# Kernel tuning notes

Measured on AMD Instinct MI355X. Metric: run time of the kernel, lower is better.

## Reference

```python
import jax, jax.numpy as jnp
import numpy as np

D = 1024        # d_model
H = 16          # query heads
HKV = 4         # kv heads (GQA)
HD = D // H     # head dim = 64
MAX_T = 1024
EPS = 1e-6
CAP = 50.0      # logit softcap


def _rope_cache(max_t, hd):
    inv = 1.0 / (10000.0 ** (np.arange(0, hd, 2, dtype=np.float32) / hd))  # (hd/2,)
    t = np.arange(max_t, dtype=np.float32)
    f = np.outer(t, inv)                                                   # (max_t, hd/2)
    return jnp.asarray(np.cos(f)), jnp.asarray(np.sin(f))


def setup_inputs() -> dict:
    key = jax.random.key(0)
    ks = jax.random.split(key, 5)
    x = jax.random.normal(ks[0], (2, 64, 256, D), jnp.float32)  # (B,T,S,D)
    wq = jax.random.normal(ks[1], (D, H * HD), jnp.float32) * 0.02
    wk = jax.random.normal(ks[2], (D, HKV * HD), jnp.float32) * 0.02
    wv = jax.random.normal(ks[3], (D, HKV * HD), jnp.float32) * 0.02
    wo = jax.random.normal(ks[4], (H * HD, D), jnp.float32) * 0.02
    q_scale = jnp.ones((HD,), jnp.float32)  # QKNorm learnable gains
    k_scale = jnp.ones((HD,), jnp.float32)
    rope_cos, rope_sin = _rope_cache(MAX_T, HD)
    return {"x": x, "wq": wq, "wk": wk, "wv": wv, "wo": wo,
            "q_scale": q_scale, "k_scale": k_scale,
            "rope_cos": rope_cos, "rope_sin": rope_sin}


def _rmsnorm(v, scale):
    return v * jax.lax.rsqrt(jnp.mean(v * v, axis=-1, keepdims=True) + EPS) * scale


def reference(x, wq, wk, wv, wo, q_scale, k_scale, rope_cos, rope_sin):
    B, T, S, Dm = x.shape
    # fold spatial positions into batch: each position attends causally over time
    xt = x.transpose(0, 2, 1, 3).reshape(B * S, T, Dm)          # (N,T,D)
    q = (xt @ wq).reshape(B * S, T, H, HD)
    k = (xt @ wk).reshape(B * S, T, HKV, HD)
    v = (xt @ wv).reshape(B * S, T, HKV, HD)
    # QK-norm (RMSNorm over head_dim) before RoPE
    q = _rmsnorm(q, q_scale)
    k = _rmsnorm(k, k_scale)
    # 1D RoPE over temporal positions (split-half convention)
    cos = rope_cos[:T][None, :, None, :]                        # (1,T,1,HD/2)
    sin = rope_sin[:T][None, :, None, :]

    def rot(u):
        u1, u2 = jnp.split(u, 2, axis=-1)
        return jnp.concatenate([u1 * cos - u2 * sin, u1 * sin + u2 * cos], axis=-1)

    q = rot(q)
    k = rot(k)
    # GQA: expand kv heads to match query heads
    rep = H // HKV
    k = jnp.repeat(k, rep, axis=2)
    v = jnp.repeat(v, rep, axis=2)
    scores = jnp.einsum('nthd,nshd->nhts', q, k) / np.float32(np.sqrt(HD))
    scores = CAP * jnp.tanh(scores / CAP)                        # logit softcap
    causal = jnp.tril(jnp.ones((T, T), bool))
    scores = jnp.where(causal, scores, jnp.float32(-1e30))
    a = jax.nn.softmax(scores, axis=-1)
    o = jnp.einsum('nhts,nshd->nthd', a, v).reshape(B * S, T, H * HD) @ wo
    return o.reshape(B, S, T, Dm).transpose(0, 2, 1, 3)          # (B,T,S,D)
```

## Files before the change

kernel.cpp:

```cpp
#include <hip/hip_runtime.h>
#include <hip/hip_bf16.h>

#define DM   1024
#define NHQ  16
#define NKVH 4
#define HDIM 64
#define TTT  64
#define SSS  256
#define NBB  2
#define MROWS 32768

using short8 = __attribute__((ext_vector_type(8))) short;
using short4v = __attribute__((ext_vector_type(4))) short;
using f32x4  = __attribute__((ext_vector_type(4))) float;

__device__ __forceinline__ short f2bf(float f) {
  union { __hip_bfloat16 h; short s; } u;
  u.h = __float2bfloat16(f);
  return u.s;
}

__device__ __forceinline__ f32x4 mfma16(short8 a, short8 b, f32x4 c) {
  return __builtin_amdgcn_mfma_f32_16x16x32_bf16(a, b, c, 0, 0, 0);
}

__device__ __forceinline__ void gload_lds16(const void* g, void* l) {
  __builtin_amdgcn_global_load_lds(
      (const __attribute__((address_space(1))) void*)g,
      (__attribute__((address_space(3))) void*)l, 16, 0, 0);
}

__global__ __launch_bounds__(256) void k_xconv(const float* __restrict__ x,
                                               short* __restrict__ xb) {
  int r = blockIdx.x;
  int n = r >> 6, t = r & 63;
  int b = n >> 8, s = n & 255;
  const float4* src = (const float4*)(x + ((size_t)((b * TTT + t) * SSS + s)) * DM);
  short4* dst = (short4*)(xb + (size_t)r * DM);
  float4 v = src[threadIdx.x];
  short4 o;
  o.x = f2bf(v.x); o.y = f2bf(v.y); o.z = f2bf(v.z); o.w = f2bf(v.w);
  dst[threadIdx.x] = o;
}

__global__ __launch_bounds__(256) void k_wtall(const float* __restrict__ wq,
                                               const float* __restrict__ wk,
                                               const float* __restrict__ wv,
                                               const float* __restrict__ wo,
                                               short* __restrict__ wqkvT,
                                               short* __restrict__ woT) {
  __shared__ float tile[32][33];
  int bid = blockIdx.x;
  const float* w; short* wt; int cols;
  if (bid < 1024)      { w = wq; wt = wqkvT; cols = 1024; }
  else if (bid < 1280) { w = wk; wt = wqkvT + (size_t)1024 * 1024; cols = 256; bid -= 1024; }
  else if (bid < 1536) { w = wv; wt = wqkvT + (size_t)1280 * 1024; cols = 256; bid -= 1280; }
  else                 { w = wo; wt = woT; cols = 1024; bid -= 1536; }
  int ctiles = cols >> 5;
  int tj = bid % ctiles;
  int td = bid / ctiles;
  int lx = threadIdx.x & 31, ly = threadIdx.x >> 5;
  #pragma unroll
  for (int rr = 0; rr < 32; rr += 8)
    tile[rr + ly][lx] = w[(size_t)(td * 32 + rr + ly) * cols + tj * 32 + lx];
  __syncthreads();
  #pragma unroll
  for (int rr = 0; rr < 32; rr += 8)
    wt[(size_t)(tj * 32 + rr + ly) * 1024 + td * 32 + lx] = f2bf(tile[lx][rr + ly]);
}

#define TILE(RAK0, RAK1, RBK0, RBK1, NLB, CLB, G, IA, IB, VM)                  \
  {                                                                            \
    short8 a[4], b0[4], b1[4];                                                 \
    _Pragma("unroll") for (int n = 0; n < 4; ++n)                              \
        b0[n] = *(const short8*)(RBK0 + n * 1024);                             \
    _Pragma("unroll") for (int m = 0; m < 4; ++m)                              \
        a[m] = *(const short8*)(RAK0 + m * 1024);                              \
    if (IA) stA0(NLB, (G + 1) * 64);                                           \
    __builtin_amdgcn_s_barrier();                                              \
    asm volatile("s_waitcnt lgkmcnt(0)" ::: "memory");                         \
    __builtin_amdgcn_s_setprio(1);                                             \
    _Pragma("unroll") for (int m = 0; m < 4; ++m)                              \
      _Pragma("unroll") for (int n = 0; n < 4; ++n)                            \
          acc[m][n] = mfma16(a[m], b0[n], acc[m][n]);                          \
    __builtin_amdgcn_s_setprio(0);                                             \
    __builtin_amdgcn_s_barrier();                                              \
    _Pragma("unroll") for (int m = 0; m < 4; ++m)                              \
        a[m] = *(const short8*)(RAK0 + 4096 + m * 1024);                       \
    if (IA) stA1(NLB, (G + 1) * 64);                                           \
    __builtin_amdgcn_s_barrier();                                              \
    asm volatile("s_waitcnt lgkmcnt(0)" ::: "memory");                         \
    __builtin_amdgcn_s_setprio(1);                                             \
    _Pragma("unroll") for (int m = 0; m < 4; ++m)                              \
      _Pragma("unroll") for (int n = 0; n < 4; ++n)                            \
          acc[4 + m][n] = mfma16(a[m], b0[n], acc[4 + m][n]);                  \
    __builtin_amdgcn_s_setprio(0);                                             \
    __builtin_amdgcn_s_barrier();                                              \
    _Pragma("unroll") for (int n = 0; n < 4; ++n)                              \
        b1[n] = *(const short8*)(RBK1 + n * 1024);                             \
    _Pragma("unroll") for (int m = 0; m < 4; ++m)                              \
        a[m] = *(const short8*)(RAK1 + m * 1024);                              \
    __builtin_amdgcn_s_barrier();                                              \
    asm volatile("s_waitcnt lgkmcnt(0)" ::: "memory");                         \
    __builtin_amdgcn_s_setprio(1);                                             \
    _Pragma("unroll") for (int m = 0; m < 4; ++m)                              \
      _Pragma("unroll") for (int n = 0; n < 4; ++n)                            \
          acc[m][n] = mfma16(a[m], b1[n], acc[m][n]);                          \
    __builtin_amdgcn_s_setprio(0);                                             \
    __builtin_amdgcn_s_barrier();                                              \
    _Pragma("unroll") for (int m = 0; m < 4; ++m)                              \
        a[m] = *(const short8*)(RAK1 + 4096 + m * 1024);                       \
    if (IB) stB(CLB, (G + 2) * 64);                                            \
    __builtin_amdgcn_s_barrier();                                              \
    asm volatile("s_waitcnt lgkmcnt(0)" ::: "memory");                         \
    __builtin_amdgcn_s_setprio(1);                                             \
    _Pragma("unroll") for (int m = 0; m < 4; ++m)                              \
      _Pragma("unroll") for (int n = 0; n < 4; ++n)                            \
          acc[4 + m][n] = mfma16(a[m], b1[n], acc[4 + m][n]);                  \
    __builtin_amdgcn_s_setprio(0);                                             \
    if (VM == 4)      asm volatile("s_waitcnt vmcnt(4)" ::: "memory");         \
    else if (VM == 0) asm volatile("s_waitcnt vmcnt(0)" ::: "memory");         \
    __builtin_amdgcn_s_barrier();                                              \
  }

__device__ __forceinline__ void gemm256(const short* __restrict__ Ab,
                                        const short* __restrict__ Bb,
                                        short* __restrict__ sm,
                                        f32x4 (&acc)[8][4]) {
  const int tid = threadIdx.x, lane = tid & 63, wid = tid >> 6;
  const int wr = wid >> 2, wc = wid & 3;
  const int ln15 = lane & 15, lhi = lane >> 4;
  const int rsw = ln15 & 7;
  const int row_t = tid >> 3;
  const int sw = ((tid & 7) ^ (row_t & 7)) << 3;
  const short* pA0 = Ab + (size_t)row_t * 1024 + sw;
  const short* pA1 = pA0 + (size_t)64 * 1024;
  const short* pA2 = pA0 + (size_t)128 * 1024;
  const short* pA3 = pA0 + (size_t)192 * 1024;
  const short* pB0 = Bb + (size_t)row_t * 1024 + sw;
  const short* pB1 = pB0 + (size_t)64 * 1024;
  const short* pB2 = pB0 + (size_t)128 * 1024;
  const short* pB3 = pB0 + (size_t)192 * 1024;
  auto stA0 = [&](short* lb, int kt) {
    gload_lds16(pA0 + kt, lb + tid * 8);
    gload_lds16(pA1 + kt, lb + 4096 + tid * 8);
  };
  auto stA1 = [&](short* lb, int kt) {
    gload_lds16(pA2 + kt, lb + 8192 + tid * 8);
    gload_lds16(pA3 + kt, lb + 12288 + tid * 8);
  };
  auto stB = [&](short* lb, int kt) {
    gload_lds16(pB0 + kt, lb + 16384 + tid * 8);
    gload_lds16(pB1 + kt, lb + 20480 + tid * 8);
    gload_lds16(pB2 + kt, lb + 24576 + tid * 8);
    gload_lds16(pB3 + kt, lb + 28672 + tid * 8);
  };
  const int sk0 = (lhi ^ rsw) << 3;
  const int sk1 = ((4 + lhi) ^ rsw) << 3;
  const short* rA0k0 = sm + (wr * 128 + ln15) * 64 + sk0;
  const short* rA0k1 = sm + (wr * 128 + ln15) * 64 + sk1;
  const short* rB0k0 = sm + 16384 + (wc * 64 + ln15) * 64 + sk0;
  const short* rB0k1 = sm + 16384 + (wc * 64 + ln15) * 64 + sk1;
  const short* rA1k0 = rA0k0 + 32768;
  const short* rA1k1 = rA0k1 + 32768;
  const short* rB1k0 = rB0k0 + 32768;
  const short* rB1k1 = rB0k1 + 32768;
  short* buf0 = sm;
  short* buf1 = sm + 32768;
  stA0(buf0, 0); stA1(buf0, 0); stB(buf0, 0);
  stA0(buf1, 64); stA1(buf1, 64); stB(buf1, 64);
  asm volatile("s_waitcnt vmcnt(8)" ::: "memory");
  __builtin_amdgcn_s_barrier();
  TILE(rA0k0, rA0k1, rB0k0, rB0k1, buf1, buf0, 0, 0, 1, 4)
  TILE(rA1k0, rA1k1, rB1k0, rB1k1, buf0, buf1, 1, 1, 1, 4)
  for (int gg = 1; gg < 7; ++gg) {
    const int g0 = gg * 2;
    TILE(rA0k0, rA0k1, rB0k0, rB0k1, buf1, buf0, g0, 1, 1, 4)
    TILE(rA1k0, rA1k1, rB1k0, rB1k1, buf0, buf1, g0 + 1, 1, 1, 4)
  }
  TILE(rA0k0, rA0k1, rB0k0, rB0k1, buf1, buf0, 14, 1, 0, 0)
  TILE(rA1k0, rA1k1, rB1k0, rB1k1, buf0, buf1, 15, 0, 0, -1)
}

__global__ __launch_bounds__(512) void k_qkv(
    const short* __restrict__ xb, const short* __restrict__ wt,
    const float* __restrict__ qscale, const float* __restrict__ kscale,
    const float* __restrict__ rcos, const float* __restrict__ rsin,
    short* __restrict__ qb, short* __restrict__ kb, short* __restrict__ vb) {
  __shared__ __align__(16) short sm[65536];
  const int bid = blockIdx.x;
  const int swz = (bid & 7) * 96 + (bid >> 3);
  const int tn = swz % 6, tm = swz / 6;
  f32x4 acc[8][4] = {};
  gemm256(xb + (size_t)tm * 256 * 1024, wt + (size_t)tn * 256 * 1024, sm, acc);

  const int tid = threadIdx.x, lane = tid & 63, wid = tid >> 6;
  const int wr = wid >> 2, wc = wid & 3;
  const int ln15 = lane & 15, lhi = lane >> 4;
  short* ot = sm;
  if (tn < 5) {
    const float* scale = (tn < 4) ? qscale : kscale;
    float sc[4];
    #pragma unroll
    for (int n = 0; n < 4; ++n) sc[n] = scale[n * 16 + ln15];
    #pragma unroll
    for (int m = 0; m < 8; ++m) {
      #pragma unroll
      for (int j = 0; j < 4; ++j) {
        float ss = 0.f;
        #pragma unroll
        for (int n = 0; n < 4; ++n) { float v = acc[m][n][j]; ss += v * v; }
        #pragma unroll
        for (int off = 8; off; off >>= 1) ss += __shfl_xor(ss, off, 64);
        float rms = rsqrtf(ss * (1.f / 64.f) + 1e-6f);
        int rl = wr * 128 + m * 16 + lhi * 4 + j;
        int t = (tm * 256 + rl) & 63;
        #pragma unroll
        for (int n = 0; n < 2; ++n) {
          int i = n * 16 + ln15;
          float cs = rcos[t * 32 + i], sn = rsin[t * 32 + i];
          float v1 = acc[m][n][j] * rms * sc[n];
          float v2 = acc[m][n + 2][j] * rms * sc[n + 2];
          ot[rl * 256 + wc * 64 + i]      = f2bf(v1 * cs - v2 * sn);
          ot[rl * 256 + wc * 64 + i + 32] = f2bf(v1 * sn + v2 * cs);
        }
      }
    }
  } else {
    #pragma unroll
    for (int m = 0; m < 8; ++m)
      #pragma unroll
      for (int n = 0; n < 4; ++n)
        #pragma unroll
        for (int j = 0; j < 4; ++j) {
          int rl = wr * 128 + m * 16 + lhi * 4 + j;
          ot[rl * 256 + wc * 64 + n * 16 + ln15] = f2bf(acc[m][n][j]);
        }
  }
  __syncthreads();
  {
    int row = tid >> 1, half = tid & 1;
    int r = tm * 256 + row;
    const uint4* src = (const uint4*)(ot + row * 256 + half * 128);
    short* dst;
    if (tn < 4)       dst = qb + (size_t)r * 1024 + tn * 256 + half * 128;
    else if (tn == 4) dst = kb + (size_t)r * 256 + half * 128;
    else              dst = vb + (size_t)r * 256 + half * 128;
    uint4* d4 = (uint4*)dst;
    #pragma unroll
    for (int i = 0; i < 16; ++i) d4[i] = src[i];
  }
}

__global__ __launch_bounds__(512) void k_attn(const short* __restrict__ qb,
                                              const short* __restrict__ kb,
                                              const short* __restrict__ vb,
                                              short* __restrict__ ob) {
  __shared__ __align__(16) short Vt[256 * 72];
  __shared__ __align__(16) short Ps[8][64 * 72];
  const int n = blockIdx.x;
  const int tid = threadIdx.x, lane = tid & 63, wid = tid >> 6;
  const int ln15 = lane & 15, lhi = lane >> 4;
  #pragma unroll
  for (int it = 0; it < 4; ++it) {
    int id = it * 512 + tid;
    int s = id >> 5, c8 = id & 31;
    short8 vv = *(const short8*)(vb + ((size_t)(n * 64 + s)) * 256 + c8 * 8);
    #pragma unroll
    for (int e = 0; e < 8; ++e) Vt[(c8 * 8 + e) * 72 + s] = vv[e];
  }
  __syncthreads();
  short* Pt = &Ps[wid][0];
  #pragma unroll
  for (int hh = 0; hh < 2; ++hh) {
    const int h = wid + hh * 8;
    const int kvh = h >> 2;
    short8 bk[4][2], aq[4][2];
    #pragma unroll
    for (int m = 0; m < 4; ++m)
      #pragma unroll
      for (int kk = 0; kk < 2; ++kk)
        bk[m][kk] = *(const short8*)(kb + ((size_t)(n * 64 + m * 16 + ln15)) * 256
                                        + kvh * 64 + kk * 32 + lhi * 8);
    #pragma unroll
    for (int nn = 0; nn < 4; ++nn)
      #pragma unroll
      for (int kk = 0; kk < 2; ++kk)
        aq[nn][kk] = *(const short8*)(qb + ((size_t)(n * 64 + nn * 16 + ln15)) * 1024
                                         + h * 64 + kk * 32 + lhi * 8);
    f32x4 sa[4][4] = {};
    __builtin_amdgcn_s_setprio(1);
    #pragma unroll
    for (int kk = 0; kk < 2; ++kk)
      #pragma unroll
      for (int m = 0; m < 4; ++m)
        #pragma unroll
        for (int nn = 0; nn < 4; ++nn)
          sa[m][nn] = mfma16(bk[m][kk], aq[nn][kk], sa[m][nn]);
    __builtin_amdgcn_s_setprio(0);
    #pragma unroll
    for (int m = 0; m < 4; ++m)
      #pragma unroll
      for (int nn = 0; nn < 4; ++nn)
        #pragma unroll
        for (int j = 0; j < 4; ++j) {
          float e2 = __expf(sa[m][nn][j] * 0.005f);
          float cap = 50.f * (e2 - 1.f) * __builtin_amdgcn_rcpf(e2 + 1.f);
          int scur = m * 16 + lhi * 4 + j, tcur = nn * 16 + ln15;
          sa[m][nn][j] = (scur <= tcur) ? cap : -1e30f;
        }
    float inv[4];
    #pragma unroll
    for (int nn = 0; nn < 4; ++nn) {
      float mx = -3e38f;
      #pragma unroll
      for (int m = 0; m < 4; ++m)
        #pragma unroll
        for (int j = 0; j < 4; ++j) mx = fmaxf(mx, sa[m][nn][j]);
      mx = fmaxf(mx, __shfl_xor(mx, 16, 64));
      mx = fmaxf(mx, __shfl_xor(mx, 32, 64));
      float sum = 0.f;
      #pragma unroll
      for (int m = 0; m < 4; ++m)
        #pragma unroll
        for (int j = 0; j < 4; ++j) {
          float e = __expf(sa[m][nn][j] - mx);
          sa[m][nn][j] = e; sum += e;
        }
      sum += __shfl_xor(sum, 16, 64);
      sum += __shfl_xor(sum, 32, 64);
      inv[nn] = __builtin_amdgcn_rcpf(sum);
    }
    #pragma unroll
    for (int nn = 0; nn < 4; ++nn)
      #pragma unroll
      for (int m = 0; m < 4; ++m) {
        short4v w;
        #pragma unroll
        for (int j = 0; j < 4; ++j) w[j] = f2bf(sa[m][nn][j] * inv[nn]);
        *(short4v*)(Pt + (nn * 16 + ln15) * 72 + m * 16 + lhi * 4) = w;
      }
    short8 ap[4][2], bv[4][2];
    #pragma unroll
    for (int m = 0; m < 4; ++m)
      #pragma unroll
      for (int kk = 0; kk < 2; ++kk)
        ap[m][kk] = *(const short8*)(Pt + (m * 16 + ln15) * 72 + kk * 32 + lhi * 8);
    #pragma unroll
    for (int nn = 0; nn < 4; ++nn)
      #pragma unroll
      for (int kk = 0; kk < 2; ++kk)
        bv[nn][kk] = *(const short8*)(&Vt[(kvh * 64 + nn * 16 + ln15) * 72 + kk * 32 + lhi * 8]);
    f32x4 oa[4][4] = {};
    __builtin_amdgcn_s_setprio(1);
    #pragma unroll
    for (int kk = 0; kk < 2; ++kk)
      #pragma unroll
      for (int m = 0; m < 4; ++m)
        #pragma unroll
        for (int nn = 0; nn < 4; ++nn)
          oa[m][nn] = mfma16(ap[m][kk], bv[nn][kk], oa[m][nn]);
    __builtin_amdgcn_s_setprio(0);
    #pragma unroll
    for (int m = 0; m < 4; ++m)
      #pragma unroll
      for (int nn = 0; nn < 4; ++nn)
        #pragma unroll
        for (int j = 0; j < 4; ++j)
          Pt[(m * 16 + lhi * 4 + j) * 72 + nn * 16 + ln15] = f2bf(oa[m][nn][j]);
    #pragma unroll
    for (int c = 0; c < 8; ++c)
      *(uint4*)(ob + ((size_t)(n * 64 + lane)) * 1024 + h * 64 + c * 8)
          = *(const uint4*)(Pt + lane * 72 + c * 8);
  }
}

__global__ __launch_bounds__(512) void k_out(const short* __restrict__ ab,
                                             const short* __restrict__ wt,
                                             float* __restrict__ out) {
  __shared__ __align__(16) short sm[65536];
  const int bid = blockIdx.x;
  const int swz = (bid & 7) * 64 + (bid >> 3);
  const int tn = swz & 3, tm = swz >> 2;
  f32x4 acc[8][4] = {};
  gemm256(ab + (size_t)tm * 256 * 1024, wt + (size_t)tn * 256 * 1024, sm, acc);

  const int tid = threadIdx.x, lane = tid & 63, wid = tid >> 6;
  const int wr = wid >> 2, wc = wid & 3;
  const int ln15 = lane & 15, lhi = lane >> 4;
  float* of = (float*)sm;
  #pragma unroll
  for (int ch = 0; ch < 2; ++ch) {
    if (wr == ch) {
      #pragma unroll
      for (int m = 0; m < 8; ++m)
        #pragma unroll
        for (int n = 0; n < 4; ++n)
          #pragma unroll
          for (int j = 0; j < 4; ++j)
            of[(m * 16 + lhi * 4 + j) * 256 + wc * 64 + n * 16 + ln15] = acc[m][n][j];
    }
    __syncthreads();
    {
      int row = tid >> 2, q4 = tid & 3;
      int r = tm * 256 + ch * 128 + row;
      int nseq = r >> 6, t = r & 63;
      int b = nseq >> 8, s = nseq & 255;
      float* dst = out + ((size_t)((b * TTT + t) * SSS + s)) * DM + tn * 256 + q4 * 64;
      const float4* src = (const float4*)(of + row * 256 + q4 * 64);
      float4* d4 = (float4*)dst;
      #pragma unroll
      for (int i = 0; i < 16; ++i) d4[i] = src[i];
    }
    __syncthreads();
  }
}

extern "C" void kernel_launch(void* const* d_in, const int* in_sizes, int n_in,
                              void* d_out, int out_size, void* d_ws, size_t ws_size,
                              hipStream_t stream) {
  const float* x  = (const float*)d_in[0];
  const float* wq = (const float*)d_in[1];
  const float* wk = (const float*)d_in[2];
  const float* wv = (const float*)d_in[3];
  const float* wo = (const float*)d_in[4];
  const float* qs = (const float*)d_in[5];
  const float* ks = (const float*)d_in[6];
  const float* rc = (const float*)d_in[7];
  const float* rs = (const float*)d_in[8];
  float* out = (float*)d_out;
  char* ws = (char*)d_ws;

  short* xb    = (short*)(ws);
  short* wqkvT = (short*)(ws + 67108864);
  short* woT   = (short*)(ws + 70254592);
  short* qb    = (short*)(ws + 72351744);
  short* kb    = (short*)(ws + 139460608);
  short* vb    = (short*)(ws + 156237824);
  short* ob    = xb;

  k_xconv<<<MROWS, 256, 0, stream>>>(x, xb);
  k_wtall<<<2560, 256, 0, stream>>>(wq, wk, wv, wo, wqkvT, woT);
  k_qkv<<<768, 512, 0, stream>>>(xb, wqkvT, qs, ks, rc, rs, qb, kb, vb);
  k_attn<<<512, 512, 0, stream>>>(qb, kb, vb, ob);
  k_out<<<512, 512, 0, stream>>>(ob, woT, out);
}
```

Baseline: 330.8 us.

## Fuse output projection into attention kernel per sequence block

Merges the separate output-projection GEMM into the attention kernel. Each block writes its 64x1024 attention output to global memory, fences, reloads it into swizzled LDS, and multiplies it by the transposed Wo, with B fragments read directly from global. This removes one kernel launch and the separate GEMM pass. In exchange, each block reads the full Wo matrix (2 MB in bf16) from global/L2 without LDS tiling, and the attention output still goes through global memory.

```diff
diff --git a/kernel.cpp b/kernel.cpp
--- a/kernel.cpp
+++ b/kernel.cpp
@@ -252,12 +252,14 @@
   }
 }
 
-__global__ __launch_bounds__(512) void k_attn(const short* __restrict__ qb,
-                                              const short* __restrict__ kb,
-                                              const short* __restrict__ vb,
-                                              short* __restrict__ ob) {
-  __shared__ __align__(16) short Vt[256 * 72];
-  __shared__ __align__(16) short Ps[8][64 * 72];
+__global__ __launch_bounds__(512, 2) void k_attn2(const short* __restrict__ qb,
+                                                  const short* __restrict__ kb,
+                                                  const short* __restrict__ vb,
+                                                  const short* __restrict__ woT,
+                                                  short* __restrict__ ob,
+                                                  float* __restrict__ out) {
+  __shared__ __align__(16) short smem[55296];
+  short* Vt = smem;
   const int n = blockIdx.x;
   const int tid = threadIdx.x, lane = tid & 63, wid = tid >> 6;
   const int ln15 = lane & 15, lhi = lane >> 4;
@@ -270,7 +272,7 @@
     for (int e = 0; e < 8; ++e) Vt[(c8 * 8 + e) * 72 + s] = vv[e];
   }
   __syncthreads();
-  short* Pt = &Ps[wid][0];
+  short* Pt = smem + 18432 + wid * 4608;
   #pragma unroll
   for (int hh = 0; hh < 2; ++hh) {
     const int h = wid + hh * 8;
@@ -373,46 +375,63 @@
       *(uint4*)(ob + ((size_t)(n * 64 + lane)) * 1024 + h * 64 + c * 8)
           = *(const uint4*)(Pt + lane * 72 + c * 8);
   }
-}
-
-__global__ __launch_bounds__(512) void k_out(const short* __restrict__ ab,
-                                             const short* __restrict__ wt,
-                                             float* __restrict__ out) {
-  __shared__ __align__(16) short sm[65536];
-  const int bid = blockIdx.x;
-  const int swz = (bid & 7) * 64 + (bid >> 3);
-  const int tn = swz & 3, tm = swz >> 2;
-  f32x4 acc[8][4] = {};
-  gemm256(ab + (size_t)tm * 256 * 1024, wt + (size_t)tn * 256 * 1024, sm, acc);
-
-  const int tid = threadIdx.x, lane = tid & 63, wid = tid >> 6;
-  const int wr = wid >> 2, wc = wid & 3;
-  const int ln15 = lane & 15, lhi = lane >> 4;
-  float* of = (float*)sm;
-  #pragma unroll
-  for (int ch = 0; ch < 2; ++ch) {
-    if (wr == ch) {
-      #pragma unroll
-      for (int m = 0; m < 8; ++m)
-        #pragma unroll
-        for (int n = 0; n < 4; ++n)
-          #pragma unroll
-          for (int j = 0; j < 4; ++j)
-            of[(m * 16 + lhi * 4 + j) * 256 + wc * 64 + n * 16 + ln15] = acc[m][n][j];
+  asm volatile("s_waitcnt vmcnt(0)" ::: "memory");
+  __threadfence();
+  __syncthreads();
+  short* Ost = smem;
+  const short* obrow = ob + (size_t)n * 64 * 1024;
+  const short* pB[8];
+  #pragma unroll
+  for (int n8 = 0; n8 < 8; ++n8)
+    pB[n8] = woT + (size_t)(wid * 128 + n8 * 16 + ln15) * 1024 + lhi * 8;
+  f32x4 c2[4][8] = {};
+  #pragma unroll
+  for (int half = 0; half < 2; ++half) {
+    #pragma unroll
+    for (int i = 0; i < 8; ++i) {
+      int id = i * 512 + tid, row = id >> 6, slot = id & 63;
+      gload_lds16(obrow + row * 1024 + half * 512 + ((slot ^ (row & 7)) << 3),
+                  Ost + id * 8);
+    }
+    asm volatile("s_waitcnt vmcnt(0)" ::: "memory");
+    __syncthreads();
+    #pragma unroll 4
+    for (int ks = 0; ks < 16; ++ks) {
+      short8 a2[4], b2[8];
+      #pragma unroll
+      for (int n8 = 0; n8 < 8; ++n8)
+        b2[n8] = *(const short8*)(pB[n8] + half * 512 + ks * 32);
+      #pragma unroll
+      for (int m = 0; m < 4; ++m)
+        a2[m] = *(const short8*)(Ost + (m * 16 + ln15) * 512
+                                     + (((ks * 4 + lhi) ^ (ln15 & 7)) << 3));
+      __builtin_amdgcn_s_setprio(1);
+      #pragma unroll
+      for (int m = 0; m < 4; ++m)
+        #pragma unroll
+        for (int n8 = 0; n8 < 8; ++n8)
+          c2[m][n8] = mfma16(a2[m], b2[n8], c2[m][n8]);
+      __builtin_amdgcn_s_setprio(0);
     }
     __syncthreads();
-    {
-      int row = tid >> 2, q4 = tid & 3;
-      int r = tm * 256 + ch * 128 + row;
-      int nseq = r >> 6, t = r & 63;
-      int b = nseq >> 8, s = nseq & 255;
-      float* dst = out + ((size_t)((b * TTT + t) * SSS + s)) * DM + tn * 256 + q4 * 64;
-      const float4* src = (const float4*)(of + row * 256 + q4 * 64);
-      float4* d4 = (float4*)dst;
-      #pragma unroll
-      for (int i = 0; i < 16; ++i) d4[i] = src[i];
+  }
+  {
+    float* slab = (float*)smem + wid * 2112;
+    const int b = n >> 8, s = n & 255;
+    int row16 = lane >> 2, q = lane & 3;
+    #pragma unroll
+    for (int m = 0; m < 4; ++m) {
+      #pragma unroll
+      for (int n8 = 0; n8 < 8; ++n8)
+        #pragma unroll
+        for (int j = 0; j < 4; ++j)
+          slab[(lhi * 4 + j) * 132 + n8 * 16 + ln15] = c2[m][n8][j];
+      int t = m * 16 + row16;
+      float* dst = out + ((size_t)((b * 64 + t) * 256 + s)) * 1024 + wid * 128 + q * 32;
+      #pragma unroll
+      for (int i2 = 0; i2 < 8; ++i2)
+        *(float4*)(dst + i2 * 4) = *(const float4*)(slab + row16 * 132 + q * 32 + i2 * 4);
     }
-    __syncthreads();
   }
 }
 
@@ -442,6 +461,5 @@
   k_xconv<<<MROWS, 256, 0, stream>>>(x, xb);
   k_wtall<<<2560, 256, 0, stream>>>(wq, wk, wv, wo, wqkvT, woT);
   k_qkv<<<768, 512, 0, stream>>>(xb, wqkvT, qs, ks, rc, rs, qb, kb, vb);
-  k_attn<<<512, 512, 0, stream>>>(qb, kb, vb, ob);
-  k_out<<<512, 512, 0, stream>>>(ob, woT, out);
-}
+  k_attn2<<<512, 512, 0, stream>>>(qb, kb, vb, woT, ob, out);
+}
```

After: 555.7 us. 1.68x slower.

## Merge prep kernels and halve attention P staging LDS for occupancy

Applied to the files above, without the earlier changes.

Combines the x-conversion and weight-transpose kernels into one launch, which removes a kernel launch and the gap between the two. In the attention kernel, the per-wave P staging buffer shrinks from 64x72 to 64x40 shorts. To fit, P@V is split into two k-halves and the output writeback into two d-halves, with launch bounds asking for more resident blocks. The aim is lower LDS use and higher occupancy, at the cost of extra LDS round trips and more registers held for the packed P values.

```diff
diff --git a/kernel.cpp b/kernel.cpp
--- a/kernel.cpp
+++ b/kernel.cpp
@@ -30,27 +30,29 @@
       (__attribute__((address_space(3))) void*)l, 16, 0, 0);
 }
 
-__global__ __launch_bounds__(256) void k_xconv(const float* __restrict__ x,
-                                               short* __restrict__ xb) {
-  int r = blockIdx.x;
-  int n = r >> 6, t = r & 63;
-  int b = n >> 8, s = n & 255;
-  const float4* src = (const float4*)(x + ((size_t)((b * TTT + t) * SSS + s)) * DM);
-  short4* dst = (short4*)(xb + (size_t)r * DM);
-  float4 v = src[threadIdx.x];
-  short4 o;
-  o.x = f2bf(v.x); o.y = f2bf(v.y); o.z = f2bf(v.z); o.w = f2bf(v.w);
-  dst[threadIdx.x] = o;
-}
-
-__global__ __launch_bounds__(256) void k_wtall(const float* __restrict__ wq,
-                                               const float* __restrict__ wk,
-                                               const float* __restrict__ wv,
-                                               const float* __restrict__ wo,
-                                               short* __restrict__ wqkvT,
-                                               short* __restrict__ woT) {
+__global__ __launch_bounds__(256) void k_prep(const float* __restrict__ x,
+                                              short* __restrict__ xb,
+                                              const float* __restrict__ wq,
+                                              const float* __restrict__ wk,
+                                              const float* __restrict__ wv,
+                                              const float* __restrict__ wo,
+                                              short* __restrict__ wqkvT,
+                                              short* __restrict__ woT) {
   __shared__ float tile[32][33];
   int bid = blockIdx.x;
+  if (bid < 32768) {
+    int r = bid;
+    int n = r >> 6, t = r & 63;
+    int b = n >> 8, s = n & 255;
+    const float4* src = (const float4*)(x + ((size_t)((b * TTT + t) * SSS + s)) * DM);
+    short4* dst = (short4*)(xb + (size_t)r * DM);
+    float4 v = src[threadIdx.x];
+    short4 o;
+    o.x = f2bf(v.x); o.y = f2bf(v.y); o.z = f2bf(v.z); o.w = f2bf(v.w);
+    dst[threadIdx.x] = o;
+    return;
+  }
+  bid -= 32768;
   const float* w; short* wt; int cols;
   if (bid < 1024)      { w = wq; wt = wqkvT; cols = 1024; }
   else if (bid < 1280) { w = wk; wt = wqkvT + (size_t)1024 * 1024; cols = 256; bid -= 1024; }
@@ -252,12 +254,12 @@
   }
 }
 
-__global__ __launch_bounds__(512) void k_attn(const short* __restrict__ qb,
-                                              const short* __restrict__ kb,
-                                              const short* __restrict__ vb,
-                                              short* __restrict__ ob) {
+__global__ __launch_bounds__(512, 4) void k_attn(const short* __restrict__ qb,
+                                                 const short* __restrict__ kb,
+                                                 const short* __restrict__ vb,
+                                                 short* __restrict__ ob) {
   __shared__ __align__(16) short Vt[256 * 72];
-  __shared__ __align__(16) short Ps[8][64 * 72];
+  __shared__ __align__(16) short Ps[8][64 * 40];
   const int n = blockIdx.x;
   const int tid = threadIdx.x, lane = tid & 63, wid = tid >> 6;
   const int ln15 = lane & 15, lhi = lane >> 4;
@@ -331,47 +333,57 @@
       sum += __shfl_xor(sum, 32, 64);
       inv[nn] = __builtin_amdgcn_rcpf(sum);
     }
-    #pragma unroll
-    for (int nn = 0; nn < 4; ++nn)
-      #pragma unroll
-      for (int m = 0; m < 4; ++m) {
+    short4v pk[4][4];
+    #pragma unroll
+    for (int m = 0; m < 4; ++m)
+      #pragma unroll
+      for (int nn = 0; nn < 4; ++nn) {
         short4v w;
         #pragma unroll
         for (int j = 0; j < 4; ++j) w[j] = f2bf(sa[m][nn][j] * inv[nn]);
-        *(short4v*)(Pt + (nn * 16 + ln15) * 72 + m * 16 + lhi * 4) = w;
+        pk[m][nn] = w;
       }
-    short8 ap[4][2], bv[4][2];
-    #pragma unroll
-    for (int m = 0; m < 4; ++m)
-      #pragma unroll
-      for (int kk = 0; kk < 2; ++kk)
-        ap[m][kk] = *(const short8*)(Pt + (m * 16 + ln15) * 72 + kk * 32 + lhi * 8);
-    #pragma unroll
-    for (int nn = 0; nn < 4; ++nn)
-      #pragma unroll
-      for (int kk = 0; kk < 2; ++kk)
-        bv[nn][kk] = *(const short8*)(&Vt[(kvh * 64 + nn * 16 + ln15) * 72 + kk * 32 + lhi * 8]);
     f32x4 oa[4][4] = {};
-    __builtin_amdgcn_s_setprio(1);
-    #pragma unroll
-    for (int kk = 0; kk < 2; ++kk)
-      #pragma unroll
-      for (int m = 0; m < 4; ++m)
+    #pragma unroll
+    for (int ks = 0; ks < 2; ++ks) {
+      #pragma unroll
+      for (int mh = 0; mh < 2; ++mh)
         #pragma unroll
         for (int nn = 0; nn < 4; ++nn)
-          oa[m][nn] = mfma16(ap[m][kk], bv[nn][kk], oa[m][nn]);
-    __builtin_amdgcn_s_setprio(0);
-    #pragma unroll
-    for (int m = 0; m < 4; ++m)
+          *(short4v*)(Pt + (nn * 16 + ln15) * 40 + mh * 16 + lhi * 4)
+              = pk[ks * 2 + mh][nn];
+      short8 ap[4], bv[4];
+      #pragma unroll
+      for (int m2 = 0; m2 < 4; ++m2)
+        ap[m2] = *(const short8*)(Pt + (m2 * 16 + ln15) * 40 + lhi * 8);
       #pragma unroll
       for (int nn = 0; nn < 4; ++nn)
-        #pragma unroll
-        for (int j = 0; j < 4; ++j)
-          Pt[(m * 16 + lhi * 4 + j) * 72 + nn * 16 + ln15] = f2bf(oa[m][nn][j]);
-    #pragma unroll
-    for (int c = 0; c < 8; ++c)
-      *(uint4*)(ob + ((size_t)(n * 64 + lane)) * 1024 + h * 64 + c * 8)
-          = *(const uint4*)(Pt + lane * 72 + c * 8);
+        bv[nn] = *(const short8*)(&Vt[(kvh * 64 + nn * 16 + ln15) * 72
+                                      + ks * 32 + lhi * 8]);
+      __builtin_amdgcn_s_setprio(1);
+      #pragma unroll
+      for (int m2 = 0; m2 < 4; ++m2)
+        #pragma unroll
+        for (int nn = 0; nn < 4; ++nn)
+          oa[m2][nn] = mfma16(ap[m2], bv[nn], oa[m2][nn]);
+      __builtin_amdgcn_s_setprio(0);
+    }
+    #pragma unroll
+    for (int dh = 0; dh < 2; ++dh) {
+      #pragma unroll
+      for (int m2 = 0; m2 < 4; ++m2)
+        #pragma unroll
+        for (int nn = 0; nn < 2; ++nn)
+          #pragma unroll
+          for (int j = 0; j < 4; ++j)
+            Pt[(m2 * 16 + lhi * 4 + j) * 40 + nn * 16 + ln15]
+                = f2bf(oa[m2][dh * 2 + nn][j]);
+      short* dst = ob + ((size_t)(n * 64 + lane)) * 1024 + h * 64 + dh * 32;
+      *(uint4*)(dst)     = *(const uint4*)(Pt + lane * 40);
+      *(uint4*)(dst + 8) = *(const uint4*)(Pt + lane * 40 + 8);
+      *(uint4*)(dst + 16) = *(const uint4*)(Pt + lane * 40 + 16);
+      *(uint4*)(dst + 24) = *(const uint4*)(Pt + lane * 40 + 24);
+    }
   }
 }
 
@@ -439,8 +451,7 @@
   short* vb    = (short*)(ws + 156237824);
   short* ob    = xb;
 
-  k_xconv<<<MROWS, 256, 0, stream>>>(x, xb);
-  k_wtall<<<2560, 256, 0, stream>>>(wq, wk, wv, wo, wqkvT, woT);
+  k_prep<<<35328, 256, 0, stream>>>(x, xb, wq, wk, wv, wo, wqkvT, woT);
   k_qkv<<<768, 512, 0, stream>>>(xb, wqkvT, qs, ks, rc, rs, qb, kb, vb);
   k_attn<<<512, 512, 0, stream>>>(qb, kb, vb, ob);
   k_out<<<512, 512, 0, stream>>>(ob, woT, out);
```

New measurement: 329.2 us. Within noise of the previous version (-0.5%).
